# Optimization experiments

Hardware: AMD Instinct MI355X
Metric: run time of the kernel (lower is better)

## Reference

```python
import jax, jax.numpy as jnp
import numpy as np

COMMIT = 0.5  # commitment from Discriminator init


def _sn(w):
    """Spectral norm, 1 power iteration from a deterministic start vector."""
    W = w.reshape(w.shape[0], -1)
    u = jnp.ones((W.shape[0],), w.dtype) / jnp.sqrt(jnp.asarray(W.shape[0], w.dtype))
    v = W.T @ u
    v = jax.lax.stop_gradient(v / (jnp.linalg.norm(v) + 1e-8))
    u2 = W @ v
    u2 = jax.lax.stop_gradient(u2 / (jnp.linalg.norm(u2) + 1e-8))
    sigma = u2 @ (W @ v)
    return w / sigma


def _conv(h, w, b, pad):
    y = jax.lax.conv_general_dilated(h, _sn(w), (1, 1), [(pad, pad), (pad, pad)],
                                     dimension_numbers=("NCHW", "OIHW", "NCHW"))
    return y + b[None, :, None, None]


def _pool(h):  # AvgPool2d(2)
    B, C, H, W = h.shape
    return h.reshape(B, C, H // 2, 2, W // 2, 2).mean(axis=(3, 5))


def _dblock(h, w1, b1, w2, b2, wsc, bsc, preact, down):
    y = jax.nn.relu(h) if preact else h
    y = _conv(y, w1, b1, 1)
    y = _conv(jax.nn.relu(y), w2, b2, 1)
    if down:
        y = _pool(y)
    sc = h
    if preact:
        if wsc is not None:
            sc = _conv(sc, wsc, bsc, 0)
        if down:
            sc = _pool(sc)
    else:
        if down:
            sc = _pool(sc)
        if wsc is not None:
            sc = _conv(sc, wsc, bsc, 0)
    return y + sc


def _quantize(h, embed):
    """VQ step (eval mode, no EMA). h: [B,C,H,W], embed: [C,K]."""
    B, C, H, W = h.shape
    xp = jnp.transpose(h, (0, 2, 3, 1))            # [B,H,W,C]
    flat = xp.reshape(-1, C)                       # [N,C]
    dist = (jnp.sum(flat ** 2, 1, keepdims=True)
            - 2.0 * flat @ embed
            + jnp.sum(embed ** 2, 0, keepdims=True))  # [N,K]
    ind = jnp.argmin(dist, axis=1)                 # [N]
    q = embed.T[ind].reshape(xp.shape)             # gather codebook rows
    diff = COMMIT * jnp.mean((jax.lax.stop_gradient(q) - xp) ** 2, axis=(1, 2, 3)).reshape(B, 1)
    q_st = xp + jax.lax.stop_gradient(q - xp)      # straight-through (unused downstream, as in source)
    K = embed.shape[1]
    probs = jnp.zeros((K,), flat.dtype).at[ind].add(1.0) / flat.shape[0]
    ppl = jnp.exp(-jnp.sum(probs * jnp.log(probs + 1e-10)))
    return jnp.transpose(q_st, (0, 3, 1, 2)), diff, ppl


def setup_inputs() -> dict:
    key = jax.random.key(0)
    ks = iter(jax.random.split(key, 40))
    d = {}
    d["x"] = jax.random.normal(next(ks), (64, 3, 32, 32), jnp.float32)
    d["y"] = jax.random.randint(next(ks), (64,), 0, 100)
    def w(shape):
        return 0.02 * jax.random.normal(next(ks), shape, jnp.float32)
    # block 0: 3->256, downsample, learnable sc
    d["b0_w1"] = w((256, 3, 3, 3));   d["b0_b1"] = jnp.zeros((256,), jnp.float32)
    d["b0_w2"] = w((256, 256, 3, 3)); d["b0_b2"] = jnp.zeros((256,), jnp.float32)
    d["b0_wsc"] = w((256, 3, 1, 1)); d["b0_bsc"] = jnp.zeros((256,), jnp.float32)
    # block 1: 256->256, downsample, learnable sc
    d["b1_w1"] = w((256, 256, 3, 3)); d["b1_b1"] = jnp.zeros((256,), jnp.float32)
    d["b1_w2"] = w((256, 256, 3, 3)); d["b1_b2"] = jnp.zeros((256,), jnp.float32)
    d["b1_wsc"] = w((256, 256, 1, 1)); d["b1_bsc"] = jnp.zeros((256,), jnp.float32)
    # blocks 2,3: 256->256, no downsample, identity sc
    d["b2_w1"] = w((256, 256, 3, 3)); d["b2_b1"] = jnp.zeros((256,), jnp.float32)
    d["b2_w2"] = w((256, 256, 3, 3)); d["b2_b2"] = jnp.zeros((256,), jnp.float32)
    d["b3_w1"] = w((256, 256, 3, 3)); d["b3_b1"] = jnp.zeros((256,), jnp.float32)
    d["b3_w2"] = w((256, 256, 3, 3)); d["b3_b2"] = jnp.zeros((256,), jnp.float32)
    # VQ codebooks: torch.randn(dim, n_embed)
    for i in range(4):
        d[f"cb{i}"] = jax.random.normal(next(ks), (256, 1024), jnp.float32)
    d["lin_w"] = w((1, 256)); d["lin_b"] = jnp.zeros((1,), jnp.float32)
    d["emb_w"] = w((100, 256))
    return d


def reference(x, y, b0_w1, b0_b1, b0_w2, b0_b2, b0_wsc, b0_bsc,
              b1_w1, b1_b1, b1_w2, b1_b2, b1_wsc, b1_bsc,
              b2_w1, b2_b1, b2_w2, b2_b2, b3_w1, b3_b1, b3_w2, b3_b2,
              cb0, cb1, cb2, cb3, lin_w, lin_b, emb_w):
    h = _dblock(x, b0_w1, b0_b1, b0_w2, b0_b2, b0_wsc, b0_bsc, preact=False, down=True)
    _, d0, _ = _quantize(h, cb0)   # quantized output discarded, as in source
    h = _dblock(h, b1_w1, b1_b1, b1_w2, b1_b2, b1_wsc, b1_bsc, preact=True, down=True)
    _, d1, _ = _quantize(h, cb1)
    h = _dblock(h, b2_w1, b2_b1, b2_w2, b2_b2, None, None, preact=True, down=False)
    _, d2, _ = _quantize(h, cb2)
    h = _dblock(h, b3_w1, b3_b1, b3_w2, b3_b2, None, None, preact=True, down=False)
    _, d3, ppl = _quantize(h, cb3)
    quant_loss = d0 + d1 + d2 + d3                 # [B,1]
    hf = jnp.sum(jax.nn.relu(h), axis=(2, 3))      # [B,256]
    out = hf @ _sn(lin_w).T + lin_b                # [B,1]
    out = out + jnp.sum(_sn(emb_w)[y] * hf, axis=1, keepdims=True)
    return (out, quant_loss, ppl)
```

## Files before the change

### kernel.cpp

```cpp
#include <hip/hip_runtime.h>
#include <math.h>

typedef __attribute__((ext_vector_type(8))) short s8v;
typedef __attribute__((ext_vector_type(4))) float f4v;

__device__ inline ushort f2bf(float x) {
    unsigned u = __float_as_uint(x);
    unsigned r = (u + 0x7FFFu + ((u >> 16) & 1u)) >> 16;
    return (ushort)r;
}
__device__ inline float bf2f(ushort h) { return __uint_as_float(((unsigned)h) << 16); }
__device__ inline float sig_of(double n2) { return (float)(n2 / (sqrt(n2) + 1e-8)); }

#define DEV __global__ __launch_bounds__(256)

struct SnMeta { const float* w[12]; int O[12]; int M[12]; };
struct SnRMap { short mat[85]; short row0[85]; };

DEV void snv2_kernel(SnMeta a, SnRMap mp, double* __restrict__ vbufraw) {
    int b = blockIdx.x;
    int id = mp.mat[b];
    int r0 = mp.row0[b];
    int O = a.O[id], M = a.M[id];
    int rend = min(r0 + 32, O);
    const float* W = a.w[id];
    for (int m = threadIdx.x; m < M; m += 256) {
        double s = 0.0;
        for (int o = r0; o < rend; ++o) s += (double)W[(size_t)o * M + m];
        atomicAdd(vbufraw + id * 2304 + m, s);
    }
}

DEV void snn_kernel(SnMeta a, const double* __restrict__ vbufraw, double* __restrict__ vnorm2) {
    int id = blockIdx.x;
    int M = a.M[id];
    double u0 = 1.0 / sqrt((double)a.O[id]);
    __shared__ double red[256];
    double ps = 0.0;
    for (int m = threadIdx.x; m < M; m += 256) { double v = vbufraw[id * 2304 + m] * u0; ps += v * v; }
    red[threadIdx.x] = ps; __syncthreads();
    for (int st = 128; st > 0; st >>= 1) { if (threadIdx.x < st) red[threadIdx.x] += red[threadIdx.x + st]; __syncthreads(); }
    if (threadIdx.x == 0) vnorm2[id] = red[0];
}

DEV void snu_kernel(SnMeta a, const double* __restrict__ vbufraw,
                    const double* __restrict__ vnorm2, double* __restrict__ unorm2) {
    int wv = blockIdx.x * 4 + (threadIdx.x >> 6);
    int lane = threadIdx.x & 63;
    const int cumR[13] = {0, 256, 512, 768, 1024, 1280, 1536, 1792, 2048, 2304, 2560, 2561, 2661};
    if (wv >= 2661) return;
    int id = 0;
    for (int i = 0; i < 12; ++i) if (wv >= cumR[i]) id = i;
    int o = wv - cumR[id];
    int M = a.M[id];
    double u0 = 1.0 / sqrt((double)a.O[id]);
    const float* Wr = a.w[id] + (size_t)o * M;
    const double* vb = vbufraw + id * 2304;
    double s = 0.0;
    for (int m = lane; m < M; m += 64) s += (double)Wr[m] * vb[m];
    for (int off = 32; off > 0; off >>= 1) s += __shfl_down(s, off, 64);
    if (lane == 0) {
        double s1 = 1.0 / (sqrt(vnorm2[id]) + 1e-8);
        double u = s * u0 * s1;
        atomicAdd(unorm2 + id, u * u);
    }
}

struct PrepArgs {
    const float* w[8]; int C[8]; int sigidx[8]; int outoff[8]; int nel[8];
    const float* cb[4];
};

DEV void prep_all_kernel(PrepArgs a, const double* __restrict__ unorm2,
                         ushort* __restrict__ wp, ushort* __restrict__ ep,
                         double* __restrict__ en64) {
    int blk = blockIdx.x;
    if (blk < 1824) {
        int gid = blk * 256 + threadIdx.x;
        int L = 0, cum = 0;
        for (int i = 0; i < 8; ++i) { int n9 = a.nel[i] / 9; if (gid >= cum && gid < cum + n9) { L = i; break; } cum += a.nel[i] / 9; }
        if (gid >= cum + a.nel[L] / 9) return;
        int e9 = gid - cum;
        int C = a.C[L];
        int NICC = (C + 31) >> 5;
        int icl = e9 & 31;
        int oc = (e9 >> 5) & 255;
        int icc = e9 >> 13;
        int ic = icc * 32 + icl;
        float inv = 1.f / sig_of(unorm2[a.sigidx[L]]);
        const float* wr = (ic < C) ? (a.w[L] + ((size_t)oc * C + ic) * 9) : nullptr;
        int nel = a.nel[L];
        int base = a.outoff[L] + icc * 8192 + oc * 32 + icl;
        #pragma unroll
        for (int tap = 0; tap < 9; ++tap) {
            float v = wr ? wr[tap] * inv : 0.f;
            ushort h = f2bf(v);
            ushort l = f2bf(v - bf2f(h));
            int o = base + tap * NICC * 8192;
            wp[o] = h;
            wp[o + nel] = l;
        }
    } else if (blk < 1824 + 4096) {
        int gid = (blk - 1824) * 256 + threadIdx.x;
        int layer = gid >> 18;
        int e = gid & 262143;
        int c5 = e & 31, k = (e >> 5) & 1023, icc = e >> 15;
        float v = a.cb[layer][(size_t)(icc * 32 + c5) * 1024 + k];
        ushort h = f2bf(v);
        ushort l = f2bf(v - bf2f(h));
        size_t o = (size_t)layer * 524288 + ((size_t)icc * 1024 + k) * 64 + c5;
        ep[o] = h; ep[o + 32] = l;
    } else {
        int b2 = blk - 1824 - 4096;
        int cc = b2 & 7, layer = b2 >> 3;
        const float* cb = a.cb[layer];
        int t = threadIdx.x;
        double d[4] = {};
        for (int c = cc * 32; c < cc * 32 + 32; ++c) {
            #pragma unroll
            for (int j = 0; j < 4; ++j) {
                double v = (double)cb[(size_t)c * 1024 + t + j * 256];
                d[j] += v * v;
            }
        }
        #pragma unroll
        for (int j = 0; j < 4; ++j) atomicAdd(en64 + layer * 1024 + t + j * 256, d[j]);
    }
}

DEV void enfin_kernel(const double* __restrict__ en64, float* __restrict__ en) {
    int gid = blockIdx.x * 256 + threadIdx.x;
    en[gid] = (float)en64[gid];
}

template<int PX>
DEV void vq2_kernel(const float* __restrict__ h, const float* __restrict__ cb,
                    const ushort* __restrict__ ep, const float* __restrict__ en,
                    float* __restrict__ dacc, int* __restrict__ hist,
                    ushort* __restrict__ hs, int HW) {
    const int MT = PX / 16;
    const int SUBS = 256 / PX;
    __shared__ ushort sA[8 * PX * 66];
    __shared__ unsigned long long sKey[PX][65];
    __shared__ int sKst[PX];
    __shared__ float sPart[PX][SUBS];
    __shared__ double sSum[PX];
    int t = threadIdx.x, wid = t >> 6, lane = t & 63, quad = lane >> 4, l15 = lane & 15;
    int pix0 = blockIdx.x * PX, n = pix0 / HW, s0 = pix0 % HW;
    const float* hb = h + (size_t)n * 256 * HW + s0;

    for (int i = t; i < 256 * PX; i += 256) {
        int c = i / PX, p = i % PX;
        float v = hb[(size_t)c * HW + p];
        ushort hv = f2bf(v), lv = f2bf(v - bf2f(hv));
        int a = (c >> 5) * (PX * 66) + p * 66 + (c & 31);
        sA[a] = hv; sA[a + 32] = lv;
    }
    __syncthreads();

    if (hs) {
        for (int i = t; i < PX * 32; i += 256) {
            int p = i >> 5; int rem = i & 31; int icc = rem >> 2, q = rem & 3;
            int aoff = icc * (PX * 66) + p * 66 + q * 8;
            s8v hv = *(const s8v*)&sA[aoff];
            s8v lv = *(const s8v*)&sA[aoff + 32];
            #pragma unroll
            for (int j = 0; j < 8; ++j) {
                float f = bf2f((ushort)hv[j]) + bf2f((ushort)lv[j]);
                if (f <= 0.f) { hv[j] = 0; lv[j] = 0; }
            }
            size_t ob = (((size_t)n * HW + s0 + p) * 8 + icc) * 64 + q * 8;
            *(s8v*)(hs + ob) = hv;
            *(s8v*)(hs + ob + 32) = lv;
        }
    }

    unsigned long long best[MT][4];
    #pragma unroll
    for (int mt = 0; mt < MT; ++mt)
        #pragma unroll
        for (int r = 0; r < 4; ++r) best[mt][r] = ~0ull;

    for (int kp = 0; kp < 2; ++kp) {
        f4v acc[MT][8];
        #pragma unroll
        for (int mt = 0; mt < MT; ++mt)
            #pragma unroll
            for (int nt = 0; nt < 8; ++nt) acc[mt][nt] = (f4v){0.f, 0.f, 0.f, 0.f};
        for (int icc = 0; icc < 8; ++icc) {
            #pragma unroll
            for (int ntc = 0; ntc < 2; ++ntc) {
                s8v eh[4], el[4];
                #pragma unroll
                for (int j = 0; j < 4; ++j) {
                    int k = wid * 256 + kp * 128 + (ntc * 4 + j) * 16 + l15;
                    const ushort* q = ep + ((size_t)icc * 1024 + k) * 64 + quad * 8;
                    eh[j] = *(const s8v*)q; el[j] = *(const s8v*)(q + 32);
                }
                #pragma unroll
                for (int mt = 0; mt < MT; ++mt) {
                    int a = icc * (PX * 66) + (mt * 16 + l15) * 66 + quad * 8;
                    s8v ah = *(const s8v*)&sA[a], al = *(const s8v*)&sA[a + 32];
                    #pragma unroll
                    for (int j = 0; j < 4; ++j) {
                        int nt = ntc * 4 + j;
                        acc[mt][nt] = __builtin_amdgcn_mfma_f32_16x16x32_bf16(al, eh[j], acc[mt][nt], 0, 0, 0);
                        acc[mt][nt] = __builtin_amdgcn_mfma_f32_16x16x32_bf16(ah, el[j], acc[mt][nt], 0, 0, 0);
                        acc[mt][nt] = __builtin_amdgcn_mfma_f32_16x16x32_bf16(ah, eh[j], acc[mt][nt], 0, 0, 0);
                    }
                }
            }
        }
        #pragma unroll
        for (int mt = 0; mt < MT; ++mt)
            #pragma unroll
            for (int nt = 0; nt < 8; ++nt) {
                int k = wid * 256 + kp * 128 + nt * 16 + l15;
                float ev = en[k];
                #pragma unroll
                for (int r = 0; r < 4; ++r) {
                    float s = ev - 2.f * acc[mt][nt][r];
                    unsigned ub = __float_as_uint(s);
                    ub = ((int)ub < 0) ? ~ub : (ub | 0x80000000u);
                    unsigned long long key = ((unsigned long long)ub << 32) | (unsigned)k;
                    if (key < best[mt][r]) best[mt][r] = key;
                }
            }
    }
    #pragma unroll
    for (int mt = 0; mt < MT; ++mt)
        #pragma unroll
        for (int r = 0; r < 4; ++r) {
            int p = mt * 16 + quad * 4 + r;
            sKey[p][wid * 16 + l15] = best[mt][r];
        }
    __syncthreads();
    if (t < PX) {
        unsigned long long m = ~0ull;
        for (int j = 0; j < 64; ++j) { unsigned long long v = sKey[t][j]; if (v < m) m = v; }
        sKst[t] = (int)(unsigned)(m & 0xFFFFFFFFu);
    }
    __syncthreads();
    {
        int p = t % PX, sub = t / PX;
        int ks = sKst[p];
        const float* ec = cb + ks;
        float d = 0.f;
        for (int c = sub * PX; c < sub * PX + PX; ++c) {
            float xv = hb[(size_t)c * HW + p];
            float evv = ec[(size_t)c * 1024];
            float df = xv - evv;
            d += df * df;
        }
        sPart[p][sub] = d;
    }
    __syncthreads();
    if (t < PX) {
        float s = 0.f;
        for (int j = 0; j < SUBS; ++j) s += sPart[t][j];
        sSum[t] = (double)s;
        if (hist) atomicAdd(hist + sKst[t], 1);
    }
    __syncthreads();
    if (t == 0) {
        double s = 0.0;
        for (int i = 0; i < PX; ++i) s += sSum[i];
        atomicAdd(dacc + n, (float)s);
    }
}

template<int ST, int NW, int NTW, int NICC, bool RELU, bool POOL, bool RES, bool INS, bool OUTS, bool SC0>
__global__ __launch_bounds__(NW * 64) void conv_mfma(
        const float* __restrict__ in, const ushort* __restrict__ ins,
        const ushort* __restrict__ wp, const float* __restrict__ bias,
        const float* __restrict__ res, float* __restrict__ out,
        ushort* __restrict__ outs, int C, int H,
        const float* __restrict__ scw, const float* __restrict__ scb,
        const double* __restrict__ un2) {
    const int MT = ST * 4;
    const int PLANE = NICC * 73728;
    const int SASZ = ST * 100 * 72;
    const int NITER = (ST * 100 * 8 + NW * 64 - 1) / (NW * 64);
    __shared__ ushort sA[(INS ? 2 : 1) * SASZ];
    __shared__ float sSC[3][16];
    int t = threadIdx.x;
    int wid = t >> 6, lane = t & 63, quad = lane >> 4, l15 = lane & 15;
    int n = blockIdx.z;
    int ocb = blockIdx.y * (NW * NTW * 16) + wid * (NTW * 16);
    int tpr = H >> 3;
    int tIdx0 = blockIdx.x * ST;

    int abase[MT];
    #pragma unroll
    for (int mt = 0; mt < MT; ++mt) {
        int m64 = (mt & 3) * 16 + l15;
        abase[mt] = (((mt >> 2) * 100 + (m64 >> 3) * 10 + (m64 & 7)) * 72) + quad * 8;
    }

    size_t gsrc[INS ? NITER : 1];
    int sdst[INS ? NITER : 1];
    s8v pref[INS ? NITER : 1];
    if (INS) {
        #pragma unroll
        for (int it = 0; it < NITER; ++it) {
            int i = t + it * NW * 64;
            gsrc[it] = (size_t)-1;
            sdst[it] = 0;
            if (i < ST * 100 * 8) {
                int pg = i >> 3, part = i & 7;
                int tile = pg / 100, pos = pg - tile * 100;
                int tIdx = tIdx0 + tile;
                int th0 = (tIdx / tpr) * 8, tw0 = (tIdx % tpr) * 8;
                int gy = th0 - 1 + pos / 10, gx = tw0 - 1 + (pos % 10);
                sdst[it] = (tile * 100 + pos) * 72 + part * 8;
                if (gy >= 0 && gy < H && gx >= 0 && gx < H)
                    gsrc[it] = ((((size_t)n * H + gy) * H + gx) * 8) * 64 + part * 8;
            }
        }
        #pragma unroll
        for (int it = 0; it < NITER; ++it)
            pref[it] = (gsrc[it] != (size_t)-1) ? *(const s8v*)(ins + gsrc[it])
                                                : (s8v){0, 0, 0, 0, 0, 0, 0, 0};
        #pragma unroll
        for (int it = 0; it < NITER; ++it) {
            int i = t + it * NW * 64;
            if (i < ST * 100 * 8) *(s8v*)(&sA[sdst[it]]) = pref[it];
        }
        if (NICC > 1) {
            #pragma unroll
            for (int it = 0; it < NITER; ++it)
                pref[it] = (gsrc[it] != (size_t)-1) ? *(const s8v*)(ins + gsrc[it] + 64)
                                                    : (s8v){0, 0, 0, 0, 0, 0, 0, 0};
        }
        __syncthreads();
    }

    f4v acc[MT][NTW];
    #pragma unroll
    for (int mt = 0; mt < MT; ++mt)
        #pragma unroll
        for (int nt = 0; nt < NTW; ++nt)
            acc[mt][nt] = (f4v){0.f, 0.f, 0.f, 0.f};

    for (int icc = 0; icc < NICC; ++icc) {
        int bufbase = INS ? (icc & 1) * SASZ : 0;
        if (INS) {
            if (icc + 1 < NICC) {
                int nb = ((icc + 1) & 1) * SASZ;
                #pragma unroll
                for (int it = 0; it < NITER; ++it) {
                    int i = t + it * NW * 64;
                    if (i < ST * 100 * 8) *(s8v*)(&sA[nb + sdst[it]]) = pref[it];
                }
                if (icc + 2 < NICC) {
                    #pragma unroll
                    for (int it = 0; it < NITER; ++it)
                        pref[it] = (gsrc[it] != (size_t)-1) ? *(const s8v*)(ins + gsrc[it] + (size_t)(icc + 2) * 64)
                                                            : (s8v){0, 0, 0, 0, 0, 0, 0, 0};
                }
            }
        } else {
            __syncthreads();
            for (int i = t; i < ST * 100 * 32; i += NW * 64) {
                int ic = i / (ST * 100);
                int rr = i - ic * (ST * 100);
                int tile = rr / 100, pos = rr - (rr / 100) * 100;
                int tIdx = tIdx0 + tile;
                int th0 = (tIdx / tpr) * 8, tw0 = (tIdx % tpr) * 8;
                int gy = th0 - 1 + pos / 10, gx = tw0 - 1 + (pos % 10);
                int gic = icc * 32 + ic;
                ushort hv = 0, lv = 0;
                if (gic < C && gy >= 0 && gy < H && gx >= 0 && gx < H) {
                    float v = in[(((size_t)n * C + gic) * H + gy) * H + gx];
                    if (RELU) v = fmaxf(v, 0.f);
                    hv = f2bf(v);
                    lv = f2bf(v - bf2f(hv));
                }
                int si = (tile * 100 + pos) * 72 + ic;
                sA[si] = hv; sA[si + 32] = lv;
            }
            __syncthreads();
        }

        s8v bh[2][NTW], bl[2][NTW];
        {
            size_t wb = (size_t)icc * 8192;
            #pragma unroll
            for (int nt = 0; nt < NTW; ++nt) {
                size_t wo = wb + (size_t)(ocb + nt * 16 + l15) * 32 + quad * 8;
                bh[0][nt] = *(const s8v*)(wp + wo);
                bl[0][nt] = *(const s8v*)(wp + PLANE + wo);
            }
        }
        #pragma unroll
        for (int tap = 0; tap < 9; ++tap) {
            int cb = tap & 1;
            if (tap < 8) {
                size_t wb = (size_t)((tap + 1) * NICC + icc) * 8192;
                #pragma unroll
                for (int nt = 0; nt < NTW; ++nt) {
                    size_t wo = wb + (size_t)(ocb + nt * 16 + l15) * 32 + quad * 8;
                    bh[cb ^ 1][nt] = *(const s8v*)(wp + wo);
                    bl[cb ^ 1][nt] = *(const s8v*)(wp + PLANE + wo);
                }
            }
            int toff = ((tap / 3) * 10 + (tap % 3)) * 72;
            #pragma unroll
            for (int mt = 0; mt < MT; ++mt) {
                s8v ah = *(const s8v*)(&sA[bufbase + abase[mt] + toff]);
                s8v al = *(const s8v*)(&sA[bufbase + abase[mt] + toff + 32]);
                #pragma unroll
                for (int nt = 0; nt < NTW; ++nt) {
                    acc[mt][nt] = __builtin_amdgcn_mfma_f32_16x16x32_bf16(al, bh[cb][nt], acc[mt][nt], 0, 0, 0);
                    acc[mt][nt] = __builtin_amdgcn_mfma_f32_16x16x32_bf16(ah, bl[cb][nt], acc[mt][nt], 0, 0, 0);
                    acc[mt][nt] = __builtin_amdgcn_mfma_f32_16x16x32_bf16(ah, bh[cb][nt], acc[mt][nt], 0, 0, 0);
                }
            }
        }
        if (INS && icc + 1 < NICC) __syncthreads();
    }

    if (SC0) {
        __syncthreads();
        if (t < 48) {
            int ic = t >> 4, p = t & 15;
            int py = p >> 2, px = p & 3;
            int th0 = (tIdx0 / tpr) * 8, tw0 = (tIdx0 % tpr) * 8;
            const float* xb = in + (((size_t)(n * 3 + ic)) * 32 + th0 + 2 * py) * 32 + tw0 + 2 * px;
            sSC[ic][p] = 0.25f * (xb[0] + xb[1] + xb[32] + xb[33]);
        }
        __syncthreads();
    }

    #pragma unroll
    for (int nt = 0; nt < NTW; ++nt) {
        int oc = ocb + nt * 16 + l15;
        float bv = bias[oc];
        #pragma unroll
        for (int mt = 0; mt < MT; ++mt) {
            int tIdx = tIdx0 + (mt >> 2);
            int th0 = (tIdx / tpr) * 8, tw0 = (tIdx % tpr) * 8;
            if (POOL) {
                float s01 = acc[mt][nt][0] + acc[mt][nt][1];
                float s23 = acc[mt][nt][2] + acc[mt][nt][3];
                float o01 = s01 + __shfl_down(s01, 32, 64);
                float o23 = s23 + __shfl_down(s23, 32, 64);
                if (quad < 2) {
                    int Ho = H >> 1;
                    int oy = (th0 >> 1) + (mt & 3);
                    int ox = (tw0 >> 1) + quad * 2;
                    size_t ob = ((size_t)(n * 256 + oc) * Ho + oy) * Ho;
                    float v0 = 0.25f * o01 + bv;
                    float v1 = 0.25f * o23 + bv;
                    if (SC0) {
                        int p0 = (mt & 3) * 4 + quad * 2;
                        float scale = 1.f / sig_of(un2[2]);
                        float sa0 = scb[oc], sa1 = scb[oc];
                        #pragma unroll
                        for (int ic = 0; ic < 3; ++ic) {
                            float wv = scw[oc * 3 + ic] * scale;
                            sa0 += sSC[ic][p0] * wv;
                            sa1 += sSC[ic][p0 + 1] * wv;
                        }
                        v0 += sa0;
                        v1 += sa1;
                    }
                    out[ob + ox] = v0;
                    out[ob + ox + 1] = v1;
                }
            } else if (OUTS) {
                int iccg = oc >> 5, ocw = oc & 31;
                #pragma unroll
                for (int r = 0; r < 4; ++r) {
                    int p16 = quad * 4 + r;
                    int y = th0 + (mt & 3) * 2 + (p16 >> 3);
                    int x = tw0 + (p16 & 7);
                    float v = fmaxf(acc[mt][nt][r] + bv, 0.f);
                    ushort h = f2bf(v);
                    size_t ob = ((((size_t)n * H + y) * H + x) * 8 + iccg) * 64;
                    outs[ob + ocw] = h;
                    outs[ob + 32 + ocw] = f2bf(v - bf2f(h));
                }
            } else {
                #pragma unroll
                for (int r = 0; r < 4; ++r) {
                    int p16 = quad * 4 + r;
                    int y = th0 + (mt & 3) * 2 + (p16 >> 3);
                    int x = tw0 + (p16 & 7);
                    size_t oi = (((size_t)(n * 256 + oc)) * H + y) * H + x;
                    float v = acc[mt][nt][r] + bv;
                    if (RES) v += res[oi];
                    out[oi] = v;
                }
            }
        }
    }
}

DEV void sc1_kernel(const float* __restrict__ h1, const float* __restrict__ wsc,
                    const float* __restrict__ bsc, const double* __restrict__ unorm2,
                    float* __restrict__ h2) {
    __shared__ float sP[64][64];
    __shared__ float sWs[64][65];
    int t = threadIdx.x;
    int n = blockIdx.x, ocb = blockIdx.y * 64;
    int ocg = t & 15, pgr = t >> 4;
    float scale = 1.f / sig_of(unorm2[5]);
    float acc[4][4] = {};
    for (int c0 = 0; c0 < 256; c0 += 64) {
        __syncthreads();
        for (int i = t; i < 4096; i += 256) {
            int ic = i >> 6, p = i & 63;
            int oh = p >> 3, ow = p & 7;
            const float* hb = h1 + (((size_t)(n * 256 + c0 + ic)) * 16 + oh * 2) * 16 + ow * 2;
            sP[ic][p] = 0.25f * (hb[0] + hb[1] + hb[16] + hb[17]);
            int oc = i >> 6, ic2 = i & 63;
            sWs[oc][ic2] = wsc[(size_t)(ocb + oc) * 256 + c0 + ic2] * scale;
        }
        __syncthreads();
        for (int ic = 0; ic < 64; ++ic) {
            float pv[4];
            #pragma unroll
            for (int q = 0; q < 4; ++q) pv[q] = sP[ic][pgr * 4 + q];
            #pragma unroll
            for (int j = 0; j < 4; ++j) {
                float wv = sWs[ocg + 16 * j][ic];
                #pragma unroll
                for (int q = 0; q < 4; ++q) acc[j][q] += wv * pv[q];
            }
        }
    }
    #pragma unroll
    for (int j = 0; j < 4; ++j) {
        int oc = ocb + ocg + 16 * j;
        float bv = bsc[oc];
        #pragma unroll
        for (int q = 0; q < 4; ++q) {
            size_t oi = ((size_t)(n * 256 + oc)) * 64 + pgr * 4 + q;
            h2[oi] += acc[j][q] + bv;
        }
    }
}

DEV void headppl_kernel(const float* __restrict__ h4, const float* __restrict__ lin_w,
                        const float* __restrict__ lin_b, const float* __restrict__ emb_w,
                        const int* __restrict__ y, const double* __restrict__ unorm2,
                        const float* __restrict__ dacc, const int* __restrict__ hist,
                        float* __restrict__ out) {
    __shared__ double r1[256], r2[256];
    int b = blockIdx.x, t = threadIdx.x;
    const float* hb = h4 + ((size_t)b * 256 + t) * 64;
    float s = 0.f;
    #pragma unroll 4
    for (int i = 0; i < 64; ++i) s += fmaxf(hb[i], 0.f);
    int yb = y[b];
    r1[t] = (double)s * (double)lin_w[t];
    r2[t] = (double)s * (double)emb_w[(size_t)yb * 256 + t];
    __syncthreads();
    for (int st = 128; st > 0; st >>= 1) { if (t < st) { r1[t] += r1[t + st]; r2[t] += r2[t + st]; } __syncthreads(); }
    if (t == 0) {
        out[b] = (float)(r1[0] / (double)sig_of(unorm2[10]) + (double)lin_b[0] + r2[0] / (double)sig_of(unorm2[11]));
        out[64 + b] = (float)(0.5 * ((double)dacc[b] * (1.0 / 65536.0)
                              + ((double)dacc[64 + b] + (double)dacc[128 + b] + (double)dacc[192 + b]) * (1.0 / 16384.0)));
    }
    if (b == 0) {
        __syncthreads();
        double ps = 0.0;
        for (int k = t; k < 1024; k += 256) {
            double p = (double)hist[k] * (1.0 / 4096.0);
            ps += p * log(p + 1e-10);
        }
        r1[t] = ps; __syncthreads();
        for (int st = 128; st > 0; st >>= 1) { if (t < st) r1[t] += r1[t + st]; __syncthreads(); }
        if (t == 0) out[128] = (float)exp(-r1[0]);
    }
}

extern "C" void kernel_launch(void* const* d_in, const int* in_sizes, int n_in,
                              void* d_out, int out_size, void* d_ws, size_t ws_size,
                              hipStream_t stream) {
    (void)in_sizes; (void)n_in; (void)out_size; (void)ws_size;
    const float* x      = (const float*)d_in[0];
    const int*   y      = (const int*)  d_in[1];
    const float* b0_w1  = (const float*)d_in[2];
    const float* b0_b1  = (const float*)d_in[3];
    const float* b0_w2  = (const float*)d_in[4];
    const float* b0_b2  = (const float*)d_in[5];
    const float* b0_wsc = (const float*)d_in[6];
    const float* b0_bsc = (const float*)d_in[7];
    const float* b1_w1  = (const float*)d_in[8];
    const float* b1_b1  = (const float*)d_in[9];
    const float* b1_w2  = (const float*)d_in[10];
    const float* b1_b2  = (const float*)d_in[11];
    const float* b1_wsc = (const float*)d_in[12];
    const float* b1_bsc = (const float*)d_in[13];
    const float* b2_w1  = (const float*)d_in[14];
    const float* b2_b1  = (const float*)d_in[15];
    const float* b2_w2  = (const float*)d_in[16];
    const float* b2_b2  = (const float*)d_in[17];
    const float* b3_w1  = (const float*)d_in[18];
    const float* b3_b1  = (const float*)d_in[19];
    const float* b3_w2  = (const float*)d_in[20];
    const float* b3_b2  = (const float*)d_in[21];
    const float* cb0    = (const float*)d_in[22];
    const float* cb1    = (const float*)d_in[23];
    const float* cb2    = (const float*)d_in[24];
    const float* cb3    = (const float*)d_in[25];
    const float* lin_w  = (const float*)d_in[26];
    const float* lin_b  = (const float*)d_in[27];
    const float* emb_w  = (const float*)d_in[28];
    float* out = (float*)d_out;

    float* wsf  = (float*)d_ws;
    float* dacc = wsf + 16;
    double* vnorm2 = (double*)(wsf + 512);
    double* unorm2 = (double*)(wsf + 544);
    int*   hist = (int*)(wsf + 1296);
    double* en64 = (double*)(wsf + 2560);
    float* en   = wsf + 10752;
    ushort* Aus  = (ushort*)(wsf + 65536);
    ushort* tbus = (ushort*)(wsf + 65536);
    ushort* t2us = (ushort*)(wsf + 4259840);
    ushort* h1s  = (ushort*)(wsf + 5308416);
    ushort* h2s  = (ushort*)(wsf + 9502720);
    ushort* h3s  = (ushort*)(wsf + 10551296);
    float* h1 = wsf + 16842752;
    float* h2 = h1 + 4194304;
    float* h3 = h2 + 1048576;
    float* h4 = h3 + 1048576;
    ushort* wp = (ushort*)(wsf + 24182784);
    double* vbufraw = (double*)(wsf + 28385280);
    ushort* ep = (ushort*)(wsf + 28440576);

    hipMemsetAsync(wsf, 0, 10752 * sizeof(float), stream);
    hipMemsetAsync(vbufraw, 0, 27648 * sizeof(double), stream);

    SnMeta sm;
    const float* sw[12] = {b0_w1, b0_w2, b0_wsc, b1_w1, b1_w2, b1_wsc,
                           b2_w1, b2_w2, b3_w1, b3_w2, lin_w, emb_w};
    int sO[12] = {256, 256, 256, 256, 256, 256, 256, 256, 256, 256, 1, 100};
    int sM[12] = {27, 2304, 3, 2304, 2304, 256, 2304, 2304, 2304, 2304, 256, 256};
    for (int i = 0; i < 12; ++i) { sm.w[i] = sw[i]; sm.O[i] = sO[i]; sm.M[i] = sM[i]; }
    SnRMap rp;
    {
        int bi = 0;
        for (int i = 0; i < 12; ++i) {
            int nb = (sO[i] + 31) / 32;
            for (int j = 0; j < nb; ++j) { rp.mat[bi] = (short)i; rp.row0[bi] = (short)(j * 32); ++bi; }
        }
    }
    snv2_kernel<<<85, 256, 0, stream>>>(sm, rp, vbufraw);
    snn_kernel<<<12, 256, 0, stream>>>(sm, vbufraw, vnorm2);
    snu_kernel<<<666, 256, 0, stream>>>(sm, vbufraw, vnorm2, unorm2);

    PrepArgs pa;
    const float* pw[8] = {b0_w1, b0_w2, b1_w1, b1_w2, b2_w1, b2_w2, b3_w1, b3_w2};
    int pC[8]   = {3, 256, 256, 256, 256, 256, 256, 256};
    int pS[8]   = {0, 1, 3, 4, 6, 7, 8, 9};
    int pOff[8] = {0, 147456, 1327104, 2506752, 3686400, 4866048, 6045696, 7225344};
    int pN[8]   = {73728, 589824, 589824, 589824, 589824, 589824, 589824, 589824};
    for (int i = 0; i < 8; ++i) { pa.w[i] = pw[i]; pa.C[i] = pC[i]; pa.sigidx[i] = pS[i]; pa.outoff[i] = pOff[i]; pa.nel[i] = pN[i]; }
    pa.cb[0] = cb0; pa.cb[1] = cb1; pa.cb[2] = cb2; pa.cb[3] = cb3;
    prep_all_kernel<<<5952, 256, 0, stream>>>(pa, unorm2, wp, ep, en64);
    enfin_kernel<<<16, 256, 0, stream>>>(en64, en);

    conv_mfma<1, 4, 2, 1, false, false, false, false, true, false><<<dim3(16, 2, 64), 256, 0, stream>>>(
        x, nullptr, wp + 0, b0_b1, nullptr, nullptr, Aus, 3, 32, nullptr, nullptr, nullptr);
    conv_mfma<1, 4, 2, 8, false, true, false, true, false, true><<<dim3(16, 2, 64), 256, 0, stream>>>(
        x, Aus, wp + 147456, b0_b2, nullptr, h1, nullptr, 256, 32, b0_wsc, b0_bsc, unorm2);
    vq2_kernel<32><<<512, 256, 0, stream>>>(h1, cb0, ep + 0, en + 0, dacc + 0, nullptr, h1s, 256);

    conv_mfma<1, 4, 1, 8, false, false, false, true, true, false><<<dim3(4, 4, 64), 256, 0, stream>>>(
        nullptr, h1s, wp + 1327104, b1_b1, nullptr, nullptr, tbus, 256, 16, nullptr, nullptr, nullptr);
    conv_mfma<1, 4, 1, 8, false, true, false, true, false, false><<<dim3(4, 4, 64), 256, 0, stream>>>(
        nullptr, tbus, wp + 2506752, b1_b2, nullptr, h2, nullptr, 256, 16, nullptr, nullptr, nullptr);
    sc1_kernel<<<dim3(64, 4), 256, 0, stream>>>(h1, b1_wsc, b1_bsc, unorm2, h2);
    vq2_kernel<16><<<256, 256, 0, stream>>>(h2, cb1, ep + 524288, en + 1024, dacc + 64, nullptr, h2s, 64);

    conv_mfma<1, 2, 1, 8, false, false, false, true, true, false><<<dim3(1, 8, 64), 128, 0, stream>>>(
        nullptr, h2s, wp + 3686400, b2_b1, nullptr, nullptr, t2us, 256, 8, nullptr, nullptr, nullptr);
    conv_mfma<1, 2, 1, 8, false, false, true, true, false, false><<<dim3(1, 8, 64), 128, 0, stream>>>(
        nullptr, t2us, wp + 4866048, b2_b2, h2, h3, nullptr, 256, 8, nullptr, nullptr, nullptr);
    vq2_kernel<16><<<256, 256, 0, stream>>>(h3, cb2, ep + 1048576, en + 2048, dacc + 128, nullptr, h3s, 64);

    conv_mfma<1, 2, 1, 8, false, false, false, true, true, false><<<dim3(1, 8, 64), 128, 0, stream>>>(
        nullptr, h3s, wp + 6045696, b3_b1, nullptr, nullptr, t2us, 256, 8, nullptr, nullptr, nullptr);
    conv_mfma<1, 2, 1, 8, false, false, true, true, false, false><<<dim3(1, 8, 64), 128, 0, stream>>>(
        nullptr, t2us, wp + 7225344, b3_b2, h3, h4, nullptr, 256, 8, nullptr, nullptr, nullptr);
    vq2_kernel<16><<<256, 256, 0, stream>>>(h4, cb3, ep + 1572864, en + 3072, dacc + 192, hist, nullptr, 64);

    headppl_kernel<<<64, 256, 0, stream>>>(h4, lin_w, lin_b, emb_w, y, unorm2, dacc, hist, out);
}
```

Measured before the change: 1.045 ms.

## Add dedicated 3-channel first conv kernel packing 27 taps into one K=32 MFMA

The first conv has only 3 input channels, yet the generic MFMA kernel padded them to a 32-wide chunk and ran it across all 9 taps. A new kernel packs the 27 (tap, channel) products into a single K=32 slice and computes each 8x8 tile with one round of split-bf16 MFMAs. The prep kernel now lays out layer-0 weights in that packed form. Separately, the generic conv kernel stores prefetch addresses as 32-bit offsets and recomputes shared-memory destinations, which should cut register pressure. The risk is 32-bit overflow if tensors grow.

```diff
diff --git a/kernel.cpp b/kernel.cpp
--- a/kernel.cpp
+++ b/kernel.cpp
@@ -81,6 +81,17 @@
         for (int i = 0; i < 8; ++i) { int n9 = a.nel[i] / 9; if (gid >= cum && gid < cum + n9) { L = i; break; } cum += a.nel[i] / 9; }
         if (gid >= cum + a.nel[L] / 9) return;
         int e9 = gid - cum;
+        if (L == 0) {
+            int oc = e9 >> 5, k = e9 & 31;
+            float inv = 1.f / sig_of(unorm2[0]);
+            float v = 0.f;
+            if (k < 27) v = a.w[0][((size_t)(oc * 3 + (k % 3))) * 9 + (k / 3)] * inv;
+            ushort h = f2bf(v);
+            ushort l = f2bf(v - bf2f(h));
+            wp[oc * 32 + k] = h;
+            wp[8192 + oc * 32 + k] = l;
+            return;
+        }
         int C = a.C[L];
         int NICC = (C + 31) >> 5;
         int icl = e9 & 31;
@@ -131,6 +142,84 @@
 DEV void enfin_kernel(const double* __restrict__ en64, float* __restrict__ en) {
     int gid = blockIdx.x * 256 + threadIdx.x;
     en[gid] = (float)en64[gid];
+}
+
+__global__ __launch_bounds__(256) void conv01k_kernel(
+        const float* __restrict__ x, const ushort* __restrict__ wp0,
+        const float* __restrict__ bias, ushort* __restrict__ outs) {
+    __shared__ float sX[3][10][10];
+    __shared__ ushort sI[64][72];
+    int t = threadIdx.x, wid = t >> 6, lane = t & 63, quad = lane >> 4, l15 = lane & 15;
+    int n = blockIdx.z;
+    int tIdx = blockIdx.x;
+    int th0 = (tIdx >> 2) * 8, tw0 = (tIdx & 3) * 8;
+    for (int i = t; i < 300; i += 256) {
+        int ch = i / 100, r = i - (i / 100) * 100;
+        int yy = r / 10, xx = r - (r / 10) * 10;
+        int gy = th0 - 1 + yy, gx = tw0 - 1 + xx;
+        float v = 0.f;
+        if (gy >= 0 && gy < 32 && gx >= 0 && gx < 32) v = x[(((size_t)n * 3 + ch) * 32 + gy) * 32 + gx];
+        sX[ch][yy][xx] = v;
+    }
+    __syncthreads();
+    for (int i = t; i < 2048; i += 256) {
+        int px = i >> 5, k = i & 31;
+        float v = 0.f;
+        if (k < 27) {
+            int tap = k / 3, ch = k - tap * 3;
+            int ty = tap / 3, tx = tap - ty * 3;
+            v = sX[ch][(px >> 3) + ty][(px & 7) + tx];
+        }
+        ushort hv = f2bf(v);
+        sI[px][k] = hv;
+        sI[px][32 + k] = f2bf(v - bf2f(hv));
+    }
+    __syncthreads();
+    int ocb = wid * 64;
+    f4v acc[4][4];
+    #pragma unroll
+    for (int mt = 0; mt < 4; ++mt)
+        #pragma unroll
+        for (int nt = 0; nt < 4; ++nt) acc[mt][nt] = (f4v){0.f, 0.f, 0.f, 0.f};
+    s8v ah[4], al[4], bh[4], bl[4];
+    #pragma unroll
+    for (int mt = 0; mt < 4; ++mt) {
+        ah[mt] = *(const s8v*)&sI[mt * 16 + l15][quad * 8];
+        al[mt] = *(const s8v*)&sI[mt * 16 + l15][32 + quad * 8];
+    }
+    #pragma unroll
+    for (int nt = 0; nt < 4; ++nt) {
+        int oc = ocb + nt * 16 + l15;
+        bh[nt] = *(const s8v*)(wp0 + oc * 32 + quad * 8);
+        bl[nt] = *(const s8v*)(wp0 + 8192 + oc * 32 + quad * 8);
+    }
+    #pragma unroll
+    for (int mt = 0; mt < 4; ++mt)
+        #pragma unroll
+        for (int nt = 0; nt < 4; ++nt) {
+            acc[mt][nt] = __builtin_amdgcn_mfma_f32_16x16x32_bf16(al[mt], bh[nt], acc[mt][nt], 0, 0, 0);
+            acc[mt][nt] = __builtin_amdgcn_mfma_f32_16x16x32_bf16(ah[mt], bl[nt], acc[mt][nt], 0, 0, 0);
+            acc[mt][nt] = __builtin_amdgcn_mfma_f32_16x16x32_bf16(ah[mt], bh[nt], acc[mt][nt], 0, 0, 0);
+        }
+    #pragma unroll
+    for (int nt = 0; nt < 4; ++nt) {
+        int oc = ocb + nt * 16 + l15;
+        float bv = bias[oc];
+        int iccg = oc >> 5, ocw = oc & 31;
+        #pragma unroll
+        for (int mt = 0; mt < 4; ++mt) {
+            #pragma unroll
+            for (int r = 0; r < 4; ++r) {
+                int px = mt * 16 + quad * 4 + r;
+                int y = th0 + (px >> 3), xx = tw0 + (px & 7);
+                float v = fmaxf(acc[mt][nt][r] + bv, 0.f);
+                ushort h = f2bf(v);
+                size_t ob = ((((size_t)n * 32 + y) * 32 + xx) * 8 + iccg) * 64;
+                outs[ob + ocw] = h;
+                outs[ob + 32 + ocw] = f2bf(v - bf2f(h));
+            }
+        }
+    }
 }
 
 template<int PX>
@@ -297,40 +386,37 @@
         abase[mt] = (((mt >> 2) * 100 + (m64 >> 3) * 10 + (m64 & 7)) * 72) + quad * 8;
     }
 
-    size_t gsrc[INS ? NITER : 1];
-    int sdst[INS ? NITER : 1];
+    unsigned gofs[INS ? NITER : 1];
     s8v pref[INS ? NITER : 1];
     if (INS) {
         #pragma unroll
         for (int it = 0; it < NITER; ++it) {
             int i = t + it * NW * 64;
-            gsrc[it] = (size_t)-1;
-            sdst[it] = 0;
+            gofs[it] = 0xFFFFFFFFu;
             if (i < ST * 100 * 8) {
                 int pg = i >> 3, part = i & 7;
                 int tile = pg / 100, pos = pg - tile * 100;
                 int tIdx = tIdx0 + tile;
                 int th0 = (tIdx / tpr) * 8, tw0 = (tIdx % tpr) * 8;
                 int gy = th0 - 1 + pos / 10, gx = tw0 - 1 + (pos % 10);
-                sdst[it] = (tile * 100 + pos) * 72 + part * 8;
                 if (gy >= 0 && gy < H && gx >= 0 && gx < H)
-                    gsrc[it] = ((((size_t)n * H + gy) * H + gx) * 8) * 64 + part * 8;
+                    gofs[it] = (unsigned)((((n * H + gy) * H + gx) * 8) * 64 + part * 8);
             }
         }
         #pragma unroll
         for (int it = 0; it < NITER; ++it)
-            pref[it] = (gsrc[it] != (size_t)-1) ? *(const s8v*)(ins + gsrc[it])
-                                                : (s8v){0, 0, 0, 0, 0, 0, 0, 0};
+            pref[it] = (gofs[it] != 0xFFFFFFFFu) ? *(const s8v*)(ins + gofs[it])
+                                                 : (s8v){0, 0, 0, 0, 0, 0, 0, 0};
         #pragma unroll
         for (int it = 0; it < NITER; ++it) {
             int i = t + it * NW * 64;
-            if (i < ST * 100 * 8) *(s8v*)(&sA[sdst[it]]) = pref[it];
+            if (i < ST * 100 * 8) *(s8v*)(&sA[(i >> 3) * 72 + (i & 7) * 8]) = pref[it];
         }
         if (NICC > 1) {
             #pragma unroll
             for (int it = 0; it < NITER; ++it)
-                pref[it] = (gsrc[it] != (size_t)-1) ? *(const s8v*)(ins + gsrc[it] + 64)
-                                                    : (s8v){0, 0, 0, 0, 0, 0, 0, 0};
+                pref[it] = (gofs[it] != 0xFFFFFFFFu) ? *(const s8v*)(ins + gofs[it] + 64)
+                                                     : (s8v){0, 0, 0, 0, 0, 0, 0, 0};
         }
         __syncthreads();
     }
@@ -350,13 +436,13 @@
                 #pragma unroll
                 for (int it = 0; it < NITER; ++it) {
                     int i = t + it * NW * 64;
-                    if (i < ST * 100 * 8) *(s8v*)(&sA[nb + sdst[it]]) = pref[it];
+                    if (i < ST * 100 * 8) *(s8v*)(&sA[nb + (i >> 3) * 72 + (i & 7) * 8]) = pref[it];
                 }
                 if (icc + 2 < NICC) {
                     #pragma unroll
                     for (int it = 0; it < NITER; ++it)
-                        pref[it] = (gsrc[it] != (size_t)-1) ? *(const s8v*)(ins + gsrc[it] + (size_t)(icc + 2) * 64)
-                                                            : (s8v){0, 0, 0, 0, 0, 0, 0, 0};
+                        pref[it] = (gofs[it] != 0xFFFFFFFFu) ? *(const s8v*)(ins + gofs[it] + (unsigned)(icc + 2) * 64)
+                                                             : (s8v){0, 0, 0, 0, 0, 0, 0, 0};
                 }
             }
         } else {
@@ -664,8 +750,7 @@
     prep_all_kernel<<<5952, 256, 0, stream>>>(pa, unorm2, wp, ep, en64);
     enfin_kernel<<<16, 256, 0, stream>>>(en64, en);
 
-    conv_mfma<1, 4, 2, 1, false, false, false, false, true, false><<<dim3(16, 2, 64), 256, 0, stream>>>(
-        x, nullptr, wp + 0, b0_b1, nullptr, nullptr, Aus, 3, 32, nullptr, nullptr, nullptr);
+    conv01k_kernel<<<dim3(16, 1, 64), 256, 0, stream>>>(x, wp, b0_b1, Aus);
     conv_mfma<1, 4, 2, 8, false, true, false, true, false, true><<<dim3(16, 2, 64), 256, 0, stream>>>(
         x, Aus, wp + 147456, b0_b2, nullptr, h1, nullptr, 256, 32, b0_wsc, b0_bsc, unorm2);
     vq2_kernel<32><<<512, 256, 0, stream>>>(h1, cb0, ep + 0, en + 0, dacc + 0, nullptr, h1s, 256);
```

Result: no change. 1.040 ms, median of 2 (-0.4%).
